# Performance work log

Hardware: AMD Instinct MI355X
Metric: run time of the kernel (lower is better)

The kernel has to match this reference:

```python
import jax, jax.numpy as jnp
import numpy as np
from itertools import product

C0, C1, C_IN, C_OUT = 16, 32, 1, 32
GRID = 768

def _enc(c):
    # injective int64 hash of 3D integer coords (values in [-4, 2043])
    return ((c[:, 0] + 4) * 2048 + (c[:, 1] + 4)) * 2048 + (c[:, 2] + 4)

def _build_km(coords, offsets):
    # kernel map for a stride-1 conv on one coordinate set:
    # per kernel offset o, pairs (in_idx, out_idx) with coords[in] == coords[out] + o
    N = coords.shape[0]
    keys = _enc(coords)
    order = np.argsort(keys)
    skeys = keys[order]
    ins, outs = [], []
    for o in offsets:
        qk = _enc(coords + np.asarray(o, np.int64))
        pos = np.searchsorted(skeys, qk)
        posc = np.clip(pos, 0, N - 1)
        valid = skeys[posc] == qk
        ins.append(order[posc[valid]].astype(np.int32))
        outs.append(np.nonzero(valid)[0].astype(np.int32))
    P = max(len(a) for a in ins)
    km_in = np.full((len(offsets), P), N, np.int32)   # pad -> zero row of x
    km_out = np.full((len(offsets), P), N, np.int32)  # pad -> dropped out row
    for k in range(len(offsets)):
        km_in[k, :len(ins[k])] = ins[k]
        km_out[k, :len(outs[k])] = outs[k]
    return km_in, km_out

def setup_inputs() -> dict:
    # voxelized surface heightfield: realistic sparse 3D point cloud occupancy
    xs, ys = np.meshgrid(np.arange(GRID), np.arange(GRID), indexing='ij')
    z = np.round(40.0 * np.sin(xs / 24.0) + 40.0 * np.cos(ys / 24.0)).astype(np.int64) + 128
    coords0 = np.stack([xs.ravel(), ys.ravel(), z.ravel()], 1).astype(np.int64)
    n0 = coords0.shape[0]
    offs27 = list(product((-1, 0, 1), repeat=3))
    km0_in, km0_out = _build_km(coords0, offs27)

    # stride-2 kernel-2 downsample: out coord = floor(c/2), offset = c mod 2
    u2 = coords0 // 2
    coords1, inv = np.unique(u2, axis=0, return_inverse=True)
    inv = inv.reshape(-1)
    n1 = coords1.shape[0]
    o = coords0 - 2 * u2
    kk = o[:, 0] * 4 + o[:, 1] * 2 + o[:, 2]
    ins, outs = [], []
    for k in range(8):
        m = np.nonzero(kk == k)[0]
        ins.append(m.astype(np.int32))
        outs.append(inv[m].astype(np.int32))
    P = max(len(a) for a in ins)
    kmd_in = np.full((8, P), n0, np.int32)
    kmd_out = np.full((8, P), n1, np.int32)
    for k in range(8):
        kmd_in[k, :len(ins[k])] = ins[k]
        kmd_out[k, :len(outs[k])] = outs[k]

    km1_in, km1_out = _build_km(coords1, offs27)

    key = jax.random.key(0)
    ks = jax.random.split(key, 6)
    w = lambda k, sh: jax.random.normal(k, sh, jnp.float32) * 0.1
    z32 = lambda c: jnp.zeros((c,), jnp.float32)
    return dict(
        in_feats=jnp.ones((n0, C_IN), jnp.float32),
        W_first=w(ks[0], (27, C_IN, C0)), b_first=z32(C0),
        W_pre=w(ks[1], (27, C0, C0)), b_pre=z32(C0),
        W_down=w(ks[2], (8, C0, C1)), b_down=z32(C1),
        W_r0=w(ks[3], (27, C1, C1)), b_r0=z32(C1),
        W_r1=w(ks[4], (27, C1, C1)), b_r1=z32(C1),
        W_fin=w(ks[5], (27, C1, C_OUT)), b_fin=z32(C_OUT),
        km0_in=jnp.asarray(km0_in), km0_out=jnp.asarray(km0_out),
        kmd_in=jnp.asarray(kmd_in), kmd_out=jnp.asarray(kmd_out),
        km1_in=jnp.asarray(km1_in), km1_out=jnp.asarray(km1_out),
        n1=int(n1),
    )

def _sparse_conv(x, W, b, km_in, km_out, n_out):
    # gather-GEMM-scatter sparse conv: out[j] += x[i] @ W[k] over pairs of offset k
    xp = jnp.concatenate([x, jnp.zeros((1, x.shape[1]), x.dtype)], 0)
    out = jnp.zeros((n_out + 1, W.shape[-1]), x.dtype)
    for k in range(W.shape[0]):  # static small loop over kernel offsets
        out = out.at[km_out[k]].add(xp[km_in[k]] @ W[k])
    return out[:n_out] + b

def reference(in_feats, W_first, b_first, W_pre, b_pre, W_down, b_down,
              W_r0, b_r0, W_r1, b_r1, W_fin, b_fin,
              km0_in, km0_out, kmd_in, kmd_out, km1_in, km1_out, n1):
    n0 = in_feats.shape[0]
    relu = jax.nn.relu
    # first_block: 3^3 conv + relu
    x = relu(_sparse_conv(in_feats, W_first, b_first, km0_in, km0_out, n0))
    cached = x  # cached_feature_list[0] (use_skip_connection=False)
    # blocks[0]: conv3x3 + relu, stride-2 downsample conv + relu
    x = relu(_sparse_conv(x, W_pre, b_pre, km0_in, km0_out, n0))
    x = relu(_sparse_conv(x, W_down, b_down, kmd_in, kmd_out, n1))
    # ResBlock
    r = relu(_sparse_conv(x, W_r0, b_r0, km1_in, km1_out, n1))
    r = _sparse_conv(r, W_r1, b_r1, km1_in, km1_out, n1)
    x = r + x
    # final conv (act=None)
    out = _sparse_conv(x, W_fin, b_fin, km1_in, km1_out, n1)
    return (out, cached)
```

## Files before the change

### kernel.cpp

```cpp
#include <hip/hip_runtime.h>


#define TPB 256

typedef __attribute__((ext_vector_type(8))) short short8;
typedef __attribute__((ext_vector_type(4))) float floatx4;

static __device__ __forceinline__ unsigned short f2b(float f) {
    union { float f; unsigned u; } v; v.f = f;
    unsigned r = v.u + 0x7fffu + ((v.u >> 16) & 1u);
    return (unsigned short)(r >> 16);
}
static __device__ __forceinline__ float b2f(unsigned short h) {
    union { unsigned u; float f; } v; v.u = ((unsigned)h) << 16;
    return v.f;
}

static __device__ __forceinline__ unsigned wave_prefix_len(
    const int* __restrict__ row, unsigned P, unsigned nv, int lane) {
    unsigned lo = 0, hi = P;
    while (hi - lo > 64u) {
        unsigned step = (hi - lo) / 64u;
        unsigned pos = lo + (unsigned)lane * step;
        bool pad = ((unsigned)row[pos] >= nv);
        unsigned long long m = __ballot(pad);
        if (m == 0ULL) {
            lo = lo + 63u * step + 1u;
        } else {
            int f = __ffsll((unsigned long long)m) - 1;
            if (f == 0) { hi = lo; break; }
            hi = lo + (unsigned)f * step;
            lo = lo + (unsigned)(f - 1) * step + 1u;
        }
    }
    unsigned span = hi - lo;
    bool pad = true;
    if ((unsigned)lane < span) pad = ((unsigned)row[lo + lane] >= nv);
    unsigned long long m = __ballot(pad);
    unsigned f = (unsigned)(__ffsll((unsigned long long)m) - 1);
    return lo + (f < span ? f : span);
}

__global__ void rowlen_k(const int* __restrict__ km0_out,
                         const int* __restrict__ km1_out,
                         const int* __restrict__ kmd_out,
                         unsigned P0, unsigned P1, unsigned Pd,
                         unsigned n0, unsigned n1, int* __restrict__ rowlen) {
    int w = (int)((blockIdx.x * blockDim.x + threadIdx.x) >> 6);
    int lane = (int)threadIdx.x & 63;
    if (w >= 62) return;
    const int* row;
    unsigned P, nv;
    if (w < 27)      { row = km0_out + (size_t)w * P0;        P = P0; nv = n0; }
    else if (w < 54) { row = km1_out + (size_t)(w - 27) * P1; P = P1; nv = n1; }
    else             { row = kmd_out + (size_t)(w - 54) * Pd; P = Pd; nv = n1; }
    unsigned len = wave_prefix_len(row, P, nv, lane);
    if (lane == 0) rowlen[w] = (int)len;
}

__global__ __launch_bounds__(TPB) void scatter_rows(
    const int* __restrict__ km0_in, const int* __restrict__ km0_out,
    const int* __restrict__ km1_in, const int* __restrict__ km1_out,
    const int* __restrict__ kmd_in, const int* __restrict__ kmd_out,
    const int* __restrict__ rowlen,
    int* __restrict__ t0, int* __restrict__ t1, int* __restrict__ td,
    unsigned P0, unsigned P1, unsigned Pd,
    unsigned rc0, unsigned rc1) {
    const int w = (int)blockIdx.y;
    const int* in;
    const int* out;
    int* tab;
    unsigned P;
    if (w < 27) {
        P = P0;
        in  = km0_in  + (size_t)w * P0;
        out = km0_out + (size_t)w * P0;
        tab = t0 + (size_t)w * rc0;
    } else if (w < 54) {
        P = P1;
        in  = km1_in  + (size_t)(w - 27) * P1;
        out = km1_out + (size_t)(w - 27) * P1;
        tab = t1 + (size_t)(w - 27) * rc1;
    } else {
        P = Pd;
        in  = kmd_in  + (size_t)(w - 54) * Pd;
        out = kmd_out + (size_t)(w - 54) * Pd;
        tab = td + (size_t)(w - 54) * rc1;
    }
    const unsigned base = blockIdx.x * (TPB * 4u);
    if (base >= P) return;
    const int len = rowlen[w];
    if ((int)base >= len) return;
    const unsigned tid = threadIdx.x;
    const unsigned Pm1 = P - 1u;
    unsigned e[4];
    int o[4], ii[4];
#pragma unroll
    for (int j = 0; j < 4; ++j) {
        e[j] = base + (unsigned)j * TPB + tid;
        unsigned ue = e[j] < P ? e[j] : Pm1;
        o[j] = out[ue];
        ii[j] = in[ue];
    }
#pragma unroll
    for (int j = 0; j < 4; ++j)
        if ((int)e[j] < len) tab[o[j]] = ii[j];
}

static __device__ __forceinline__ void pack16_elem(
    const float* __restrict__ W, unsigned short* __restrict__ Wp,
    int t, int COUT, int Ksrc) {
    int j = t & 7;
    int r = t >> 3;
    int n = r % COUT; r /= COUT;
    int q = r & 3;
    int k2 = r >> 2;
    int ks = 2 * k2 + (q >> 1);
    int cin = (q & 1) * 8 + j;
    float v = (ks < Ksrc) ? W[(ks * 16 + cin) * COUT + n] : 0.f;
    Wp[t] = f2b(v);
}

__global__ void pack_all(const float* __restrict__ W_pre, const float* __restrict__ W_down,
                         const float* __restrict__ W_r0, const float* __restrict__ W_r1,
                         const float* __restrict__ W_fin,
                         unsigned short* __restrict__ wp_pre, unsigned short* __restrict__ wp_down,
                         unsigned short* __restrict__ wp_r0, unsigned short* __restrict__ wp_r1,
                         unsigned short* __restrict__ wp_fin,
                         unsigned short* p0, unsigned short* p1, unsigned short* p2,
                         unsigned short* p3, unsigned short* p4) {
    int t = blockIdx.x * blockDim.x + threadIdx.x;
    if (t < 7168) { pack16_elem(W_pre, wp_pre, t, 16, 27); return; }
    t -= 7168;
    if (t < 4096) { pack16_elem(W_down, wp_down, t, 32, 8); return; }
    t -= 4096;
    if (t < 27648) {
        int j = t & 7, n = (t >> 3) & 31, q = (t >> 8) & 3, k = t >> 10;
        wp_r0[t] = f2b(W_r0[(k * 32 + q * 8 + j) * 32 + n]); return;
    }
    t -= 27648;
    if (t < 27648) {
        int j = t & 7, n = (t >> 3) & 31, q = (t >> 8) & 3, k = t >> 10;
        wp_r1[t] = f2b(W_r1[(k * 32 + q * 8 + j) * 32 + n]); return;
    }
    t -= 27648;
    if (t < 27648) {
        int j = t & 7, n = (t >> 3) & 31, q = (t >> 8) & 3, k = t >> 10;
        wp_fin[t] = f2b(W_fin[(k * 32 + q * 8 + j) * 32 + n]); return;
    }
    t -= 27648;
    if (t < 16) p0[t] = 0;
    else if (t < 32) p1[t - 16] = 0;
    else if (t < 64) p2[t - 32] = 0;
    else if (t < 96) p3[t - 64] = 0;
    else if (t < 128) p4[t - 96] = 0;
}

__global__ __launch_bounds__(TPB) void conv_first_k(
    const float* __restrict__ xin, const float* __restrict__ W,
    const float* __restrict__ b, const int* __restrict__ tab, long long rowcap,
    int n0, float* __restrict__ outf, unsigned short* __restrict__ outb) {
    int j = blockIdx.x * blockDim.x + threadIdx.x;
    if (j >= n0) return;
    float acc[16];
#pragma unroll
    for (int c = 0; c < 16; ++c) acc[c] = b[c];
#pragma unroll
    for (int k = 0; k < 27; ++k) {
        int idx = tab[(long long)k * rowcap + j];
        bool ok = (unsigned)idx < (unsigned)n0;
        int cidx = ok ? idx : 0;
        float v = xin[cidx];
        v = ok ? v : 0.f;
        const float* Wk = W + k * 16;
#pragma unroll
        for (int c = 0; c < 16; ++c) acc[c] = fmaf(v, Wk[c], acc[c]);
    }
    float* orow = outf + (long long)j * 16;
    unsigned short* brow = outb + (long long)j * 16;
#pragma unroll
    for (int c = 0; c < 16; ++c) {
        float v = fmaxf(acc[c], 0.f);
        orow[c] = v;
        brow[c] = f2b(v);
    }
}

template <int CIN, int COUT, int NT, int SB, int SE>
static __device__ __forceinline__ void kchunk(
    const unsigned short* __restrict__ xb, const unsigned short* __restrict__ Wp,
    const int* __restrict__ tab, long long rowcap, int n_in,
    long long j0, int m, int q, int coff, floatx4 (&acc)[4][NT]) {
    constexpr int NS = SE - SB;
    if (NS <= 0) return;
    int idx[NS > 0 ? NS : 1][4];
#pragma unroll
    for (int s = 0; s < NS; ++s) {
        const int ks = (CIN == 32) ? (SB + s) : 2 * (SB + s) + (q >> 1);
        const int* trow = tab + (long long)ks * rowcap + j0 + m;
#pragma unroll
        for (int t = 0; t < 4; ++t) {
            unsigned v = (unsigned)trow[16 * t];
            idx[s][t] = (int)(v < (unsigned)n_in ? v : (unsigned)n_in);
        }
    }
    short8 cur[4];
#pragma unroll
    for (int t = 0; t < 4; ++t)
        cur[t] = *(const short8*)(xb + (long long)idx[0][t] * CIN + coff);
#pragma unroll
    for (int s = 0; s < NS; ++s) {
        short8 nxt[4];
        if (s + 1 < NS) {
#pragma unroll
            for (int t = 0; t < 4; ++t)
                nxt[t] = *(const short8*)(xb + (long long)idx[s + 1][t] * CIN + coff);
        }
        short8 b0 = *(const short8*)(Wp + ((((SB + s) * 4 + q) * COUT) + m) * 8);
        short8 b1;
        if (NT == 2) b1 = *(const short8*)(Wp + ((((SB + s) * 4 + q) * COUT) + 16 + m) * 8);
#pragma unroll
        for (int t = 0; t < 4; ++t) {
            acc[t][0] = __builtin_amdgcn_mfma_f32_16x16x32_bf16(cur[t], b0, acc[t][0], 0, 0, 0);
            if (NT == 2)
                acc[t][1] = __builtin_amdgcn_mfma_f32_16x16x32_bf16(cur[t], b1, acc[t][1], 0, 0, 0);
        }
        if (s + 1 < NS) {
#pragma unroll
            for (int t = 0; t < 4; ++t) cur[t] = nxt[t];
        }
    }
}

template <int CIN, int COUT, int STEPS, bool RELU, bool RES, bool WF32, bool WB16>
__global__ __launch_bounds__(TPB, 4) void conv_mfma(
    const unsigned short* __restrict__ xb,
    const unsigned short* __restrict__ Wp,
    const float* __restrict__ bias,
    const int* __restrict__ tab, long long rowcap, int n_in, int n_out,
    long long ntiles,
    const unsigned short* __restrict__ resb,
    float* __restrict__ outf, unsigned short* __restrict__ outb) {
    constexpr int NT = COUT / 16;
    __shared__ floatx4 red[NT][12 * 64];
    int runs = (int)gridDim.x >> 3;
    long long tile = (long long)((blockIdx.x & 7) * runs + (blockIdx.x >> 3));
    if (tile >= ntiles) return;
    int wv = (int)((threadIdx.x >> 6) & 3);
    int lane = (int)threadIdx.x & 63;
    int m = lane & 15, q = lane >> 4;
    long long j0 = tile * 64;

    floatx4 acc[4][NT];
#pragma unroll
    for (int t = 0; t < 4; ++t)
#pragma unroll
        for (int nt = 0; nt < NT; ++nt) acc[t][nt] = floatx4{0.f, 0.f, 0.f, 0.f};

    const int coff = (CIN == 32) ? q * 8 : (q & 1) * 8;
    constexpr int C1 = STEPS / 4, C2 = STEPS / 2, C3 = (3 * STEPS) / 4;
    if (wv == 0)
        kchunk<CIN, COUT, NT, 0, C1>(xb, Wp, tab, rowcap, n_in, j0, m, q, coff, acc);
    else if (wv == 1)
        kchunk<CIN, COUT, NT, C1, C2>(xb, Wp, tab, rowcap, n_in, j0, m, q, coff, acc);
    else if (wv == 2)
        kchunk<CIN, COUT, NT, C2, C3>(xb, Wp, tab, rowcap, n_in, j0, m, q, coff, acc);
    else
        kchunk<CIN, COUT, NT, C3, STEPS>(xb, Wp, tab, rowcap, n_in, j0, m, q, coff, acc);

#pragma unroll
    for (int t = 0; t < 4; ++t) {
        if (t != wv) {
            int sl = wv * 3 + (t > wv ? t - 1 : t);
#pragma unroll
            for (int nt = 0; nt < NT; ++nt)
                red[nt][sl * 64 + lane] = acc[t][nt];
        }
    }
    floatx4 own[NT];
#pragma unroll
    for (int nt = 0; nt < NT; ++nt) own[nt] = acc[0][nt];
#pragma unroll
    for (int t = 1; t < 4; ++t)
#pragma unroll
        for (int nt = 0; nt < NT; ++nt)
            if (wv == t) own[nt] = acc[t][nt];
    __syncthreads();
#pragma unroll
    for (int w = 0; w < 4; ++w) {
        if (w != wv) {
            int sl = w * 3 + (wv > w ? wv - 1 : wv);
#pragma unroll
            for (int nt = 0; nt < NT; ++nt)
                own[nt] += red[nt][sl * 64 + lane];
        }
    }

    float bs[2];
    bs[0] = bias[m];
    if (NT == 2) bs[1] = bias[16 + m];
    long long jb = j0 + wv * 16;
#pragma unroll
    for (int u = 0; u < 4; ++u) {
        long long r = jb + q * 4 + u;
        if (r < n_out) {
#pragma unroll
            for (int nt = 0; nt < NT; ++nt) {
                float v = own[nt][u] + bs[nt];
                if (RES) v += b2f(resb[r * COUT + nt * 16 + m]);
                if (RELU) v = fmaxf(v, 0.f);
                if (WF32) outf[r * COUT + nt * 16 + m] = v;
                if (WB16) outb[r * COUT + nt * 16 + m] = f2b(v);
            }
        }
    }
}

static inline unsigned nblk(long long n, int b) { return (unsigned)((n + b - 1) / b); }
static inline unsigned pad8(unsigned g) { return ((g + 7) / 8) * 8; }
static inline size_t align64(size_t x) { return (x + 63) & ~(size_t)63; }

extern "C" void kernel_launch(void* const* d_in, const int* in_sizes, int n_in_cnt,
                              void* d_out, int out_size, void* d_ws, size_t ws_size,
                              hipStream_t stream) {
    const float* in_feats = (const float*)d_in[0];
    const float* W_first = (const float*)d_in[1];
    const float* b_first = (const float*)d_in[2];
    const float* W_pre   = (const float*)d_in[3];
    const float* b_pre   = (const float*)d_in[4];
    const float* W_down  = (const float*)d_in[5];
    const float* b_down  = (const float*)d_in[6];
    const float* W_r0    = (const float*)d_in[7];
    const float* b_r0    = (const float*)d_in[8];
    const float* W_r1    = (const float*)d_in[9];
    const float* b_r1    = (const float*)d_in[10];
    const float* W_fin   = (const float*)d_in[11];
    const float* b_fin   = (const float*)d_in[12];
    const int* km0_in  = (const int*)d_in[13];
    const int* km0_out = (const int*)d_in[14];
    const int* kmd_in  = (const int*)d_in[15];
    const int* kmd_out = (const int*)d_in[16];
    const int* km1_in  = (const int*)d_in[17];
    const int* km1_out = (const int*)d_in[18];

    const int n0 = in_sizes[0];
    const int n1 = (out_size - 16 * n0) / 32;
    const long long P0 = in_sizes[13] / 27;
    const long long Pd = in_sizes[15] / 8;
    const long long P1 = in_sizes[17] / 27;

    const long long rc0 = ((n0 + 64) / 64) * 64;
    const long long rc1 = ((n1 + 64) / 64) * 64;
    const long long T0 = rc0 / 64, T1 = rc1 / 64;

    float* out_lo = (float*)d_out;
    float* cached = out_lo + (size_t)n1 * 32;

    char* base = (char*)d_ws;
    size_t off = 0;
    auto alloc = [&](size_t bytes) { void* p = base + off; off = align64(off + bytes); return p; };
    int* t0 = (int*)alloc(sizeof(int) * 28 * rc0);
    int* t1 = (int*)alloc(sizeof(int) * 27 * rc1);
    int* td = (int*)alloc(sizeof(int) * 8 * rc1);
    unsigned short* c0b   = (unsigned short*)alloc(sizeof(short) * 16 * (n0 + 1));
    unsigned short* x0pre = (unsigned short*)alloc(sizeof(short) * 16 * (n0 + 1));
    unsigned short* x1a   = (unsigned short*)alloc(sizeof(short) * 32 * (n1 + 1));
    unsigned short* x1b   = (unsigned short*)alloc(sizeof(short) * 32 * (n1 + 1));
    unsigned short* x1c   = (unsigned short*)alloc(sizeof(short) * 32 * (n1 + 1));
    unsigned short* wp_pre  = (unsigned short*)alloc(sizeof(short) * 14 * 4 * 16 * 8);
    unsigned short* wp_down = (unsigned short*)alloc(sizeof(short) * 4 * 4 * 32 * 8);
    unsigned short* wp_r0   = (unsigned short*)alloc(sizeof(short) * 27 * 1024);
    unsigned short* wp_r1   = (unsigned short*)alloc(sizeof(short) * 27 * 1024);
    unsigned short* wp_fin  = (unsigned short*)alloc(sizeof(short) * 27 * 1024);
    int* rowlen = (int*)alloc(sizeof(int) * 64);
    (void)ws_size; (void)n_in_cnt;

    rowlen_k<<<16, TPB, 0, stream>>>(km0_out, km1_out, kmd_out,
                                     (unsigned)P0, (unsigned)P1, (unsigned)Pd,
                                     (unsigned)n0, (unsigned)n1, rowlen);

    long long maxP = P0 > P1 ? P0 : P1;
    if (Pd > maxP) maxP = Pd;
    dim3 sgrid(nblk(maxP, TPB * 4), 62);
    scatter_rows<<<sgrid, TPB, 0, stream>>>(
        km0_in, km0_out, km1_in, km1_out, kmd_in, kmd_out, rowlen,
        t0, t1, td, (unsigned)P0, (unsigned)P1, (unsigned)Pd,
        (unsigned)rc0, (unsigned)rc1);

    const long long packN = 7168 + 4096 + 3 * 27648 + 128;
    pack_all<<<nblk(packN, TPB), TPB, 0, stream>>>(
        W_pre, W_down, W_r0, W_r1, W_fin,
        wp_pre, wp_down, wp_r0, wp_r1, wp_fin,
        c0b + (size_t)n0 * 16, x0pre + (size_t)n0 * 16,
        x1a + (size_t)n1 * 32, x1b + (size_t)n1 * 32, x1c + (size_t)n1 * 32);

    conv_first_k<<<nblk(n0, TPB), TPB, 0, stream>>>(in_feats, W_first, b_first, t0, rc0,
                                                    n0, cached, c0b);
    const unsigned g0 = pad8((unsigned)T0), g1 = pad8((unsigned)T1);
    conv_mfma<16, 16, 14, true, false, false, true><<<g0, TPB, 0, stream>>>(
        c0b, wp_pre, b_pre, t0, rc0, n0, n0, T0, nullptr, nullptr, x0pre);
    conv_mfma<16, 32, 4, true, false, false, true><<<g1, TPB, 0, stream>>>(
        x0pre, wp_down, b_down, td, rc1, n0, n1, T1, nullptr, nullptr, x1a);
    conv_mfma<32, 32, 27, true, false, false, true><<<g1, TPB, 0, stream>>>(
        x1a, wp_r0, b_r0, t1, rc1, n1, n1, T1, nullptr, nullptr, x1b);
    conv_mfma<32, 32, 27, false, true, false, true><<<g1, TPB, 0, stream>>>(
        x1b, wp_r1, b_r1, t1, rc1, n1, n1, T1, x1a, nullptr, x1c);
    conv_mfma<32, 32, 27, false, false, true, false><<<g1, TPB, 0, stream>>>(
        x1c, wp_fin, b_fin, t1, rc1, n1, n1, T1, nullptr, out_lo, nullptr);
}
```

Measured before the change: 468.9 us.

## Replace dense scatter tables with CSR tile offsets built by binary search

Drops the dense per-offset output-to-input tables for the 27-offset maps and the pass that scatters into them. Instead, a binary search over the sorted km_out rows finds per-64-row tile start offsets, and each conv block rebuilds its local index table in shared memory from the pair lists. The downsample map scatter is folded into the weight-pack kernel. This removes large table writes and reads, at the cost of an extra shared-memory fill per tile and a reliance on km_out being sorted per offset.

```diff
diff --git a/kernel.cpp b/kernel.cpp
--- a/kernel.cpp
+++ b/kernel.cpp
@@ -16,95 +16,39 @@
     return v.f;
 }
 
-static __device__ __forceinline__ unsigned wave_prefix_len(
-    const int* __restrict__ row, unsigned P, unsigned nv, int lane) {
-    unsigned lo = 0, hi = P;
-    while (hi - lo > 64u) {
-        unsigned step = (hi - lo) / 64u;
-        unsigned pos = lo + (unsigned)lane * step;
-        bool pad = ((unsigned)row[pos] >= nv);
-        unsigned long long m = __ballot(pad);
-        if (m == 0ULL) {
-            lo = lo + 63u * step + 1u;
-        } else {
-            int f = __ffsll((unsigned long long)m) - 1;
-            if (f == 0) { hi = lo; break; }
-            hi = lo + (unsigned)f * step;
-            lo = lo + (unsigned)(f - 1) * step + 1u;
-        }
-    }
-    unsigned span = hi - lo;
-    bool pad = true;
-    if ((unsigned)lane < span) pad = ((unsigned)row[lo + lane] >= nv);
-    unsigned long long m = __ballot(pad);
-    unsigned f = (unsigned)(__ffsll((unsigned long long)m) - 1);
-    return lo + (f < span ? f : span);
-}
-
-__global__ void rowlen_k(const int* __restrict__ km0_out,
+__global__ void search_k(const int* __restrict__ km0_out,
                          const int* __restrict__ km1_out,
-                         const int* __restrict__ kmd_out,
-                         unsigned P0, unsigned P1, unsigned Pd,
-                         unsigned n0, unsigned n1, int* __restrict__ rowlen) {
-    int w = (int)((blockIdx.x * blockDim.x + threadIdx.x) >> 6);
-    int lane = (int)threadIdx.x & 63;
-    if (w >= 62) return;
+                         long long P0, long long P1, int T0, int T1,
+                         int n0, int n1,
+                         int* __restrict__ st0, int* __restrict__ st1) {
+    unsigned t = blockIdx.x * blockDim.x + threadIdx.x;
+    unsigned N0 = 27u * (unsigned)(T0 + 1);
+    unsigned N1 = 27u * (unsigned)(T1 + 1);
     const int* row;
-    unsigned P, nv;
-    if (w < 27)      { row = km0_out + (size_t)w * P0;        P = P0; nv = n0; }
-    else if (w < 54) { row = km1_out + (size_t)(w - 27) * P1; P = P1; nv = n1; }
-    else             { row = kmd_out + (size_t)(w - 54) * Pd; P = Pd; nv = n1; }
-    unsigned len = wave_prefix_len(row, P, nv, lane);
-    if (lane == 0) rowlen[w] = (int)len;
-}
-
-__global__ __launch_bounds__(TPB) void scatter_rows(
-    const int* __restrict__ km0_in, const int* __restrict__ km0_out,
-    const int* __restrict__ km1_in, const int* __restrict__ km1_out,
-    const int* __restrict__ kmd_in, const int* __restrict__ kmd_out,
-    const int* __restrict__ rowlen,
-    int* __restrict__ t0, int* __restrict__ t1, int* __restrict__ td,
-    unsigned P0, unsigned P1, unsigned Pd,
-    unsigned rc0, unsigned rc1) {
-    const int w = (int)blockIdx.y;
-    const int* in;
-    const int* out;
-    int* tab;
-    unsigned P;
-    if (w < 27) {
-        P = P0;
-        in  = km0_in  + (size_t)w * P0;
-        out = km0_out + (size_t)w * P0;
-        tab = t0 + (size_t)w * rc0;
-    } else if (w < 54) {
-        P = P1;
-        in  = km1_in  + (size_t)(w - 27) * P1;
-        out = km1_out + (size_t)(w - 27) * P1;
-        tab = t1 + (size_t)(w - 27) * rc1;
+    long long P;
+    int th;
+    int* dst;
+    if (t < N0) {
+        unsigned k = t / (unsigned)(T0 + 1), tile = t - k * (unsigned)(T0 + 1);
+        row = km0_out + (long long)k * P0; P = P0;
+        long long thr = (long long)tile * 64;
+        th = thr < n0 ? (int)thr : n0;
+        dst = st0 + t;
     } else {
-        P = Pd;
-        in  = kmd_in  + (size_t)(w - 54) * Pd;
-        out = kmd_out + (size_t)(w - 54) * Pd;
-        tab = td + (size_t)(w - 54) * rc1;
-    }
-    const unsigned base = blockIdx.x * (TPB * 4u);
-    if (base >= P) return;
-    const int len = rowlen[w];
-    if ((int)base >= len) return;
-    const unsigned tid = threadIdx.x;
-    const unsigned Pm1 = P - 1u;
-    unsigned e[4];
-    int o[4], ii[4];
-#pragma unroll
-    for (int j = 0; j < 4; ++j) {
-        e[j] = base + (unsigned)j * TPB + tid;
-        unsigned ue = e[j] < P ? e[j] : Pm1;
-        o[j] = out[ue];
-        ii[j] = in[ue];
-    }
-#pragma unroll
-    for (int j = 0; j < 4; ++j)
-        if ((int)e[j] < len) tab[o[j]] = ii[j];
+        t -= N0;
+        if (t >= N1) return;
+        unsigned k = t / (unsigned)(T1 + 1), tile = t - k * (unsigned)(T1 + 1);
+        row = km1_out + (long long)k * P1; P = P1;
+        long long thr = (long long)tile * 64;
+        th = thr < n1 ? (int)thr : n1;
+        dst = st1 + t;
+    }
+    long long lo = 0, hi = P;
+    while (lo < hi) {
+        long long mid = (lo + hi) >> 1;
+        if (row[mid] < th) lo = mid + 1; else hi = mid;
+    }
+    *dst = (int)lo;
 }
 
 static __device__ __forceinline__ void pack16_elem(
@@ -121,7 +65,9 @@
     Wp[t] = f2b(v);
 }
 
-__global__ void pack_all(const float* __restrict__ W_pre, const float* __restrict__ W_down,
+__global__ void prep_all(const int* __restrict__ kmd_in, const int* __restrict__ kmd_out,
+                         int* __restrict__ td, unsigned Pd, unsigned rc1, unsigned n1,
+                         const float* __restrict__ W_pre, const float* __restrict__ W_down,
                          const float* __restrict__ W_r0, const float* __restrict__ W_r1,
                          const float* __restrict__ W_fin,
                          unsigned short* __restrict__ wp_pre, unsigned short* __restrict__ wp_down,
@@ -129,7 +75,15 @@
                          unsigned short* __restrict__ wp_fin,
                          unsigned short* p0, unsigned short* p1, unsigned short* p2,
                          unsigned short* p3, unsigned short* p4) {
-    int t = blockIdx.x * blockDim.x + threadIdx.x;
+    unsigned tu = blockIdx.x * blockDim.x + threadIdx.x;
+    unsigned Nd = 8u * Pd;
+    if (tu < Nd) {
+        int o = kmd_out[tu];
+        int i = kmd_in[tu];
+        if ((unsigned)o < n1) td[(tu / Pd) * rc1 + (unsigned)o] = i;
+        return;
+    }
+    int t = (int)(tu - Nd);
     if (t < 7168) { pack16_elem(W_pre, wp_pre, t, 16, 27); return; }
     t -= 7168;
     if (t < 4096) { pack16_elem(W_down, wp_down, t, 32, 8); return; }
@@ -158,17 +112,36 @@
 
 __global__ __launch_bounds__(TPB) void conv_first_k(
     const float* __restrict__ xin, const float* __restrict__ W,
-    const float* __restrict__ b, const int* __restrict__ tab, long long rowcap,
+    const float* __restrict__ b,
+    const int* __restrict__ km_in, const int* __restrict__ km_out,
+    const int* __restrict__ st, long long P, int T,
     int n0, float* __restrict__ outf, unsigned short* __restrict__ outb) {
-    int j = blockIdx.x * blockDim.x + threadIdx.x;
+    __shared__ int lidx[27][256];
+    const int blk = (int)blockIdx.x;
+    const int j0 = blk * 256;
+    const int wv = (int)(threadIdx.x >> 6), lane = (int)(threadIdx.x & 63);
+    const int ta = 4 * blk;
+    const int tb = (4 * blk + 4 < T) ? 4 * blk + 4 : T;
+    for (int r = wv; r < 27; r += 4) {
+#pragma unroll
+        for (int i = 0; i < 4; ++i) lidx[r][lane + 64 * i] = n0;
+        int s = st[r * (T + 1) + ta];
+        int e = st[r * (T + 1) + tb];
+        for (int i = s + lane; i < e; i += 64) {
+            int o = km_out[(long long)r * P + i];
+            lidx[r][o - j0] = km_in[(long long)r * P + i];
+        }
+    }
+    __syncthreads();
+    int j = j0 + (int)threadIdx.x;
     if (j >= n0) return;
     float acc[16];
 #pragma unroll
     for (int c = 0; c < 16; ++c) acc[c] = b[c];
 #pragma unroll
     for (int k = 0; k < 27; ++k) {
-        int idx = tab[(long long)k * rowcap + j];
-        bool ok = (unsigned)idx < (unsigned)n0;
+        int idx = lidx[k][threadIdx.x];
+        bool ok = idx < n0;
         int cidx = ok ? idx : 0;
         float v = xin[cidx];
         v = ok ? v : 0.f;
@@ -186,10 +159,10 @@
     }
 }
 
-template <int CIN, int COUT, int NT, int SB, int SE>
+template <int CIN, int COUT, int NT, int SB, int SE, bool CSR>
 static __device__ __forceinline__ void kchunk(
     const unsigned short* __restrict__ xb, const unsigned short* __restrict__ Wp,
-    const int* __restrict__ tab, long long rowcap, int n_in,
+    const int* __restrict__ tab, long long rowcap, const int* lidx, int n_in,
     long long j0, int m, int q, int coff, floatx4 (&acc)[4][NT]) {
     constexpr int NS = SE - SB;
     if (NS <= 0) return;
@@ -197,11 +170,15 @@
 #pragma unroll
     for (int s = 0; s < NS; ++s) {
         const int ks = (CIN == 32) ? (SB + s) : 2 * (SB + s) + (q >> 1);
-        const int* trow = tab + (long long)ks * rowcap + j0 + m;
 #pragma unroll
         for (int t = 0; t < 4; ++t) {
-            unsigned v = (unsigned)trow[16 * t];
-            idx[s][t] = (int)(v < (unsigned)n_in ? v : (unsigned)n_in);
+            if (CSR) {
+                idx[s][t] = lidx[ks * 64 + 16 * t + m];
+            } else {
+                const int* trow = tab + (long long)ks * rowcap + j0 + m;
+                unsigned v = (unsigned)trow[16 * t];
+                idx[s][t] = (int)(v < (unsigned)n_in ? v : (unsigned)n_in);
+            }
         }
     }
     short8 cur[4];
@@ -232,17 +209,51 @@
     }
 }
 
-template <int CIN, int COUT, int STEPS, bool RELU, bool RES, bool WF32, bool WB16>
+template <int CIN, int COUT, int NT, int SB, int SE, bool CSR>
+static __device__ __forceinline__ void chunk_run(
+    const unsigned short* __restrict__ xb, const unsigned short* __restrict__ Wp,
+    const int* __restrict__ km_in, const int* __restrict__ km_out,
+    const int* __restrict__ st, int T, long long P,
+    const int* __restrict__ tab, long long rowcap,
+    int n_in, long long j0, int tile, int lane, int m, int q, int coff,
+    int* lidx, floatx4 (&acc)[4][NT]) {
+    if (CSR) {
+        constexpr int R0 = (CIN == 32) ? SB : 2 * SB;
+        constexpr int R1 = (CIN == 32) ? SE : 2 * SE;
+#pragma unroll
+        for (int r = R0; r < R1; ++r) lidx[r * 64 + lane] = n_in;
+#pragma unroll
+        for (int r = R0; r < R1; ++r) {
+            if (r < 27) {
+                int s = st[r * (T + 1) + tile];
+                int e = st[r * (T + 1) + tile + 1];
+                int i = s + lane;
+                if (i < e) {
+                    int o = km_out[(long long)r * P + i];
+                    lidx[r * 64 + (o - (int)j0)] = km_in[(long long)r * P + i];
+                }
+            }
+        }
+    }
+    kchunk<CIN, COUT, NT, SB, SE, CSR>(xb, Wp, tab, rowcap, lidx, n_in,
+                                       CSR ? 0 : j0, m, q, coff, acc);
+}
+
+template <int CIN, int COUT, int STEPS, bool CSR, bool RELU, bool RES, bool WF32, bool WB16>
 __global__ __launch_bounds__(TPB, 4) void conv_mfma(
     const unsigned short* __restrict__ xb,
     const unsigned short* __restrict__ Wp,
     const float* __restrict__ bias,
-    const int* __restrict__ tab, long long rowcap, int n_in, int n_out,
-    long long ntiles,
+    const int* __restrict__ km_in, const int* __restrict__ km_out,
+    const int* __restrict__ st, int T, long long P,
+    const int* __restrict__ tab, long long rowcap,
+    int n_in, int n_out, long long ntiles,
     const unsigned short* __restrict__ resb,
     float* __restrict__ outf, unsigned short* __restrict__ outb) {
     constexpr int NT = COUT / 16;
+    constexpr int NR = (CIN == 16) ? 2 * STEPS : STEPS;
     __shared__ floatx4 red[NT][12 * 64];
+    __shared__ int lidx[CSR ? NR * 64 : 64];
     int runs = (int)gridDim.x >> 3;
     long long tile = (long long)((blockIdx.x & 7) * runs + (blockIdx.x >> 3));
     if (tile >= ntiles) return;
@@ -260,13 +271,17 @@
     const int coff = (CIN == 32) ? q * 8 : (q & 1) * 8;
     constexpr int C1 = STEPS / 4, C2 = STEPS / 2, C3 = (3 * STEPS) / 4;
     if (wv == 0)
-        kchunk<CIN, COUT, NT, 0, C1>(xb, Wp, tab, rowcap, n_in, j0, m, q, coff, acc);
+        chunk_run<CIN, COUT, NT, 0, C1, CSR>(xb, Wp, km_in, km_out, st, T, P, tab, rowcap,
+                                             n_in, j0, (int)tile, lane, m, q, coff, lidx, acc);
     else if (wv == 1)
-        kchunk<CIN, COUT, NT, C1, C2>(xb, Wp, tab, rowcap, n_in, j0, m, q, coff, acc);
+        chunk_run<CIN, COUT, NT, C1, C2, CSR>(xb, Wp, km_in, km_out, st, T, P, tab, rowcap,
+                                              n_in, j0, (int)tile, lane, m, q, coff, lidx, acc);
     else if (wv == 2)
-        kchunk<CIN, COUT, NT, C2, C3>(xb, Wp, tab, rowcap, n_in, j0, m, q, coff, acc);
+        chunk_run<CIN, COUT, NT, C2, C3, CSR>(xb, Wp, km_in, km_out, st, T, P, tab, rowcap,
+                                              n_in, j0, (int)tile, lane, m, q, coff, lidx, acc);
     else
-        kchunk<CIN, COUT, NT, C3, STEPS>(xb, Wp, tab, rowcap, n_in, j0, m, q, coff, acc);
+        chunk_run<CIN, COUT, NT, C3, STEPS, CSR>(xb, Wp, km_in, km_out, st, T, P, tab, rowcap,
+                                                 n_in, j0, (int)tile, lane, m, q, coff, lidx, acc);
 
 #pragma unroll
     for (int t = 0; t < 4; ++t) {
@@ -349,9 +364,9 @@
     const long long Pd = in_sizes[15] / 8;
     const long long P1 = in_sizes[17] / 27;
 
+    const long long rc1 = ((n1 + 64) / 64) * 64;
     const long long rc0 = ((n0 + 64) / 64) * 64;
-    const long long rc1 = ((n1 + 64) / 64) * 64;
-    const long long T0 = rc0 / 64, T1 = rc1 / 64;
+    const int T0 = (int)(rc0 / 64), T1 = (int)(rc1 / 64);
 
     float* out_lo = (float*)d_out;
     float* cached = out_lo + (size_t)n1 * 32;
@@ -359,9 +374,9 @@
     char* base = (char*)d_ws;
     size_t off = 0;
     auto alloc = [&](size_t bytes) { void* p = base + off; off = align64(off + bytes); return p; };
-    int* t0 = (int*)alloc(sizeof(int) * 28 * rc0);
-    int* t1 = (int*)alloc(sizeof(int) * 27 * rc1);
     int* td = (int*)alloc(sizeof(int) * 8 * rc1);
+    int* st0 = (int*)alloc(sizeof(int) * 27 * (T0 + 1));
+    int* st1 = (int*)alloc(sizeof(int) * 27 * (T1 + 1));
     unsigned short* c0b   = (unsigned short*)alloc(sizeof(short) * 16 * (n0 + 1));
     unsigned short* x0pre = (unsigned short*)alloc(sizeof(short) * 16 * (n0 + 1));
     unsigned short* x1a   = (unsigned short*)alloc(sizeof(short) * 32 * (n1 + 1));
@@ -372,39 +387,37 @@
     unsigned short* wp_r0   = (unsigned short*)alloc(sizeof(short) * 27 * 1024);
     unsigned short* wp_r1   = (unsigned short*)alloc(sizeof(short) * 27 * 1024);
     unsigned short* wp_fin  = (unsigned short*)alloc(sizeof(short) * 27 * 1024);
-    int* rowlen = (int*)alloc(sizeof(int) * 64);
     (void)ws_size; (void)n_in_cnt;
 
-    rowlen_k<<<16, TPB, 0, stream>>>(km0_out, km1_out, kmd_out,
-                                     (unsigned)P0, (unsigned)P1, (unsigned)Pd,
-                                     (unsigned)n0, (unsigned)n1, rowlen);
-
-    long long maxP = P0 > P1 ? P0 : P1;
-    if (Pd > maxP) maxP = Pd;
-    dim3 sgrid(nblk(maxP, TPB * 4), 62);
-    scatter_rows<<<sgrid, TPB, 0, stream>>>(
-        km0_in, km0_out, km1_in, km1_out, kmd_in, kmd_out, rowlen,
-        t0, t1, td, (unsigned)P0, (unsigned)P1, (unsigned)Pd,
-        (unsigned)rc0, (unsigned)rc1);
-
-    const long long packN = 7168 + 4096 + 3 * 27648 + 128;
-    pack_all<<<nblk(packN, TPB), TPB, 0, stream>>>(
+    const long long searchN = 27LL * (T0 + 1) + 27LL * (T1 + 1);
+    search_k<<<nblk(searchN, TPB), TPB, 0, stream>>>(
+        km0_out, km1_out, P0, P1, T0, T1, n0, n1, st0, st1);
+
+    const long long prepN = 8 * Pd + 7168 + 4096 + 3 * 27648 + 128;
+    prep_all<<<nblk(prepN, TPB), TPB, 0, stream>>>(
+        kmd_in, kmd_out, td, (unsigned)Pd, (unsigned)rc1, (unsigned)n1,
         W_pre, W_down, W_r0, W_r1, W_fin,
         wp_pre, wp_down, wp_r0, wp_r1, wp_fin,
         c0b + (size_t)n0 * 16, x0pre + (size_t)n0 * 16,
         x1a + (size_t)n1 * 32, x1b + (size_t)n1 * 32, x1c + (size_t)n1 * 32);
 
-    conv_first_k<<<nblk(n0, TPB), TPB, 0, stream>>>(in_feats, W_first, b_first, t0, rc0,
-                                                    n0, cached, c0b);
+    conv_first_k<<<nblk(n0, TPB), TPB, 0, stream>>>(
+        in_feats, W_first, b_first, km0_in, km0_out, st0, P0, T0, n0, cached, c0b);
+
     const unsigned g0 = pad8((unsigned)T0), g1 = pad8((unsigned)T1);
-    conv_mfma<16, 16, 14, true, false, false, true><<<g0, TPB, 0, stream>>>(
-        c0b, wp_pre, b_pre, t0, rc0, n0, n0, T0, nullptr, nullptr, x0pre);
-    conv_mfma<16, 32, 4, true, false, false, true><<<g1, TPB, 0, stream>>>(
-        x0pre, wp_down, b_down, td, rc1, n0, n1, T1, nullptr, nullptr, x1a);
-    conv_mfma<32, 32, 27, true, false, false, true><<<g1, TPB, 0, stream>>>(
-        x1a, wp_r0, b_r0, t1, rc1, n1, n1, T1, nullptr, nullptr, x1b);
-    conv_mfma<32, 32, 27, false, true, false, true><<<g1, TPB, 0, stream>>>(
-        x1b, wp_r1, b_r1, t1, rc1, n1, n1, T1, x1a, nullptr, x1c);
-    conv_mfma<32, 32, 27, false, false, true, false><<<g1, TPB, 0, stream>>>(
-        x1c, wp_fin, b_fin, t1, rc1, n1, n1, T1, nullptr, out_lo, nullptr);
-}
+    conv_mfma<16, 16, 14, true, true, false, false, true><<<g0, TPB, 0, stream>>>(
+        c0b, wp_pre, b_pre, km0_in, km0_out, st0, T0, P0, nullptr, 0,
+        n0, n0, T0, nullptr, nullptr, x0pre);
+    conv_mfma<16, 32, 4, false, true, false, false, true><<<g1, TPB, 0, stream>>>(
+        x0pre, wp_down, b_down, nullptr, nullptr, nullptr, 0, 0, td, rc1,
+        n0, n1, T1, nullptr, nullptr, x1a);
+    conv_mfma<32, 32, 27, true, true, false, false, true><<<g1, TPB, 0, stream>>>(
+        x1a, wp_r0, b_r0, km1_in, km1_out, st1, T1, P1, nullptr, 0,
+        n1, n1, T1, nullptr, nullptr, x1b);
+    conv_mfma<32, 32, 27, true, false, true, false, true><<<g1, TPB, 0, stream>>>(
+        x1b, wp_r1, b_r1, km1_in, km1_out, st1, T1, P1, nullptr, 0,
+        n1, n1, T1, x1a, nullptr, x1c);
+    conv_mfma<32, 32, 27, true, false, false, true, false><<<g1, TPB, 0, stream>>>(
+        x1c, wp_fin, b_fin, km1_in, km1_out, st1, T1, P1, nullptr, 0,
+        n1, n1, T1, nullptr, out_lo, nullptr);
+}
```

New measurement: 471.3 us. Within noise of the previous version (+0.5%).
